# Kernel optimization log

Measured on AMD Instinct MI355X. Metric: run time of the kernel, lower is better.

The kernel has to match this reference:

```python
import jax, jax.numpy as jnp
import numpy as np


def setup_inputs() -> dict:
    key = jax.random.key(0)
    k1, k2 = jax.random.split(key)
    img_render_points = jax.random.normal(k1, (128, 128, 2), dtype=jnp.float32)
    ref_catheter_contour_point_cloud = jax.random.normal(k2, (16384, 2), dtype=jnp.float32)
    return {
        "img_render_points": img_render_points,
        "ref_catheter_contour_point_cloud": ref_catheter_contour_point_cloud,
    }


def reference(img_render_points, ref_catheter_contour_point_cloud):
    # Flatten to point cloud (N, 2)
    pc = img_render_points.reshape(-1, 2)
    ref = ref_catheter_contour_point_cloud  # (M, 2)
    # Pairwise Euclidean distances (N, M); torch.norm(..., dim=2) equivalent
    diff = pc[:, None, :] - ref[None, :, :]          # (N, M, 2)
    distances = jnp.sqrt(jnp.sum(diff * diff, axis=-1))  # (N, M)
    min_d1 = jnp.min(distances, axis=1)  # nearest ref point for each render point
    min_d2 = jnp.min(distances, axis=0)  # nearest render point for each ref point
    chamfer_loss = jnp.sum(min_d1) + jnp.sum(min_d2)
    return chamfer_loss
```

## Files before the change

### kernel.cpp

```cpp
#include <hip/hip_runtime.h>
#include <math.h>

#define NPTS 16384
#define G    64
#define NB   (G * G)
#define CAP  128
#define OCAP 2048
#define BV   5.0f
#define H    0.15625f
#define INVH (1.0f / H)
#define SLICE 1160


__global__ __launch_bounds__(256) void k_zero(unsigned int* __restrict__ cnt,
                                              float* __restrict__ out) {
    int i = blockIdx.x * 256 + threadIdx.x;
    if (i < 2 * NB + 2) cnt[i] = 0u;
    if (i == 0) out[0] = 0.0f;
}

__global__ __launch_bounds__(256) void k_scatter(
        const float2* __restrict__ pc, const float2* __restrict__ ref,
        unsigned int* __restrict__ cnt, unsigned int* __restrict__ ovf_cnt,
        float2* __restrict__ binned, float2* __restrict__ ovf) {
    int t  = blockIdx.x * 256 + threadIdx.x;
    int cl = t >> 14;
    int i  = t & (NPTS - 1);
    float2 p = (cl ? ref : pc)[i];
    int bx = (int)floorf((p.x + BV) * INVH); bx = min(max(bx, 0), G - 1);
    int by = (int)floorf((p.y + BV) * INVH); by = min(max(by, 0), G - 1);
    int b = cl * NB + by * G + bx;
    unsigned idx = atomicAdd(&cnt[b], 1u);
    if (idx < CAP) {
        binned[(size_t)b * CAP + idx] = p;
    } else {
        unsigned oi = atomicAdd(&ovf_cnt[cl], 1u);
        if (oi < OCAP) ovf[cl * OCAP + oi] = p;
    }
}

__global__ __launch_bounds__(256) void k_query(
        const float2* __restrict__ pc, const float2* __restrict__ ref,
        const unsigned int* __restrict__ cnt, const unsigned int* __restrict__ ovf_cnt,
        const float2* __restrict__ binned, const float2* __restrict__ ovf,
        float* __restrict__ out) {
    __shared__ float2 s_pts[4 * SLICE];
    __shared__ float  s_bsum[4];

    int d    = blockIdx.y;
    int td   = 1 - d;
    int wave = threadIdx.x >> 6;
    int lane = threadIdx.x & 63;
    int w    = blockIdx.x * 4 + wave;
    float2* my = s_pts + wave * SLICE;
    float sum = 0.0f;

    if (w < NB) {
        int c  = (w * 65) & (NB - 1);
        int cx = c & (G - 1), cy = c >> 6;
        int nq = (int)min(cnt[d * NB + c], (unsigned)CAP);
        if (nq > 0) {
            const unsigned int* tcnt = cnt + td * NB;
            const float2* tbin = binned + (size_t)td * NB * CAP;
            unsigned novf = min(ovf_cnt[td], (unsigned)OCAP);

            int nt = 0;
#pragma unroll
            for (int dy = -1; dy <= 1; ++dy) {
#pragma unroll
                for (int dx = -1; dx <= 1; ++dx) {
                    int x = cx + dx, y = cy + dy;
                    if ((unsigned)x < G && (unsigned)y < G) {
                        int t  = y * G + x;
                        int tn = (int)min(tcnt[t], (unsigned)CAP);
                        for (int i = lane; i < tn; i += 64)
                            my[nt + i] = tbin[(size_t)t * CAP + i];
                        nt += tn;
                    }
                }
            }
            int ntr = (nt + 3) & ~3;
            if (lane < ntr - nt) my[nt + lane] = make_float2(1e30f, 1e30f);

            for (int base = 0; base < nq; base += 64) {
                bool valid = (base + lane) < nq;
                float2 q = valid ? binned[((size_t)(d * NB + c)) * CAP + base + lane]
                                 : make_float2(0.0f, 0.0f);
                float best = valid ? INFINITY : 0.0f;

                for (unsigned j = 0; j < novf; ++j) {
                    float2 tp = ovf[td * OCAP + j];
                    float ddx = q.x - tp.x, ddy = q.y - tp.y;
                    best = fminf(best, fmaf(ddx, ddx, ddy * ddy));
                }

                const float4* p4 = (const float4*)my;
#pragma unroll 4
                for (int k = 0; k < ntr; k += 4) {
                    float4 ab = p4[k >> 1];
                    float4 cd = p4[(k >> 1) + 1];
                    float dx0 = q.x - ab.x, dy0 = q.y - ab.y;
                    float dx1 = q.x - ab.z, dy1 = q.y - ab.w;
                    float dx2 = q.x - cd.x, dy2 = q.y - cd.y;
                    float dx3 = q.x - cd.z, dy3 = q.y - cd.w;
                    float d0 = fmaf(dx0, dx0, dy0 * dy0);
                    float d1 = fmaf(dx1, dx1, dy1 * dy1);
                    float d2 = fmaf(dx2, dx2, dy2 * dy2);
                    float d3 = fmaf(dx3, dx3, dy3 * dy3);
                    best = fminf(best, fminf(fminf(d0, d1), fminf(d2, d3)));
                }

                for (int r = 2; r < G; ++r) {
                    float bnd = (float)(r - 1) * H;
                    if (__all(best <= bnd * bnd)) break;
                    int ncells = 8 * r;
                    for (int k0 = 0; k0 < ncells; k0 += 64) {
                        int k = k0 + lane;
                        int t = 0, tn = 0;
                        if (k < ncells) {
                            int side = (k >= 6 * r) ? 3 : (k >= 4 * r) ? 2 :
                                       (k >= 2 * r) ? 1 : 0;
                            int i = k - side * 2 * r;
                            int x, y;
                            if      (side == 0) { y = cy - r; x = cx - r + i; }
                            else if (side == 1) { x = cx + r; y = cy - r + i; }
                            else if (side == 2) { y = cy + r; x = cx + r - i; }
                            else                { x = cx - r; y = cy + r - i; }
                            if ((unsigned)x < G && (unsigned)y < G) {
                                t  = y * G + x;
                                tn = (int)min(tcnt[t], (unsigned)CAP);
                            }
                        }
                        unsigned long long mask = __ballot(tn > 0);
                        while (mask) {
                            int src = __builtin_ctzll(mask);
                            mask &= mask - 1;
                            int tt  = __shfl(t,  src, 64);
                            int ttn = __shfl(tn, src, 64);
                            const float2* tp = tbin + (size_t)tt * CAP;
                            for (int j = 0; j < ttn; ++j) {
                                float2 pt = tp[j];
                                float ddx = q.x - pt.x, ddy = q.y - pt.y;
                                best = fminf(best, fmaf(ddx, ddx, ddy * ddy));
                            }
                        }
                    }
                }
                if (valid) sum += sqrtf(best);
            }
        }
    } else if (w == NB) {
        unsigned n = min(ovf_cnt[d], (unsigned)OCAP);
        const float2* tgt = d ? pc : ref;
        for (unsigned i = lane; i < n; i += 64) {
            float2 q = ovf[d * OCAP + i];
            float best = INFINITY;
            for (int j = 0; j < NPTS; ++j) {
                float2 tp = tgt[j];
                float ddx = q.x - tp.x, ddy = q.y - tp.y;
                best = fminf(best, fmaf(ddx, ddx, ddy * ddy));
            }
            sum += sqrtf(best);
        }
    }

#pragma unroll
    for (int off = 32; off > 0; off >>= 1)
        sum += __shfl_down(sum, off, 64);
    if (lane == 0) s_bsum[wave] = sum;
    __syncthreads();
    if (threadIdx.x == 0) {
        float t = s_bsum[0] + s_bsum[1] + s_bsum[2] + s_bsum[3];
        if (t != 0.0f) atomicAdd(out, t);
    }
}

extern "C" void kernel_launch(void* const* d_in, const int* in_sizes, int n_in,
                              void* d_out, int out_size, void* d_ws, size_t ws_size,
                              hipStream_t stream) {
    const float2* pc  = (const float2*)d_in[0];
    const float2* ref = (const float2*)d_in[1];
    float* out = (float*)d_out;

    char* w = (char*)d_ws;
    unsigned int* cnt     = (unsigned int*)(w);
    unsigned int* ovf_cnt = (unsigned int*)(w + 32768);
    float2*       binned  = (float2*)(w + 65536);
    float2*       ovf     = (float2*)(w + 65536 +
                              (size_t)2 * NB * CAP * sizeof(float2));

    k_zero<<<(2 * NB + 2 + 255) / 256, 256, 0, stream>>>(cnt, out);
    k_scatter<<<(2 * NPTS) / 256, 256, 0, stream>>>(pc, ref, cnt, ovf_cnt, binned, ovf);
    k_query<<<dim3(1025, 2), 256, 0, stream>>>(pc, ref, cnt, ovf_cnt, binned, ovf, out);
}
```

Baseline: 102.6 us.

## Process two query points per lane and stage ring cells into LDS

Measured after the change: 88.86 us. 1.15x faster.

```diff
diff --git a/kernel.cpp b/kernel.cpp
--- a/kernel.cpp
+++ b/kernel.cpp
@@ -10,6 +10,7 @@
 #define H    0.15625f
 #define INVH (1.0f / H)
 #define SLICE 1160
+#define WCAP  1152
 
 
 __global__ __launch_bounds__(256) void k_zero(unsigned int* __restrict__ cnt,
@@ -64,90 +65,116 @@
             const float2* tbin = binned + (size_t)td * NB * CAP;
             unsigned novf = min(ovf_cnt[td], (unsigned)OCAP);
 
-            int nt = 0;
-#pragma unroll
-            for (int dy = -1; dy <= 1; ++dy) {
+            int tid9[9], tn9[9], nv = 0;
+#pragma unroll
+            for (int dy = -1; dy <= 1; ++dy)
 #pragma unroll
                 for (int dx = -1; dx <= 1; ++dx) {
                     int x = cx + dx, y = cy + dy;
                     if ((unsigned)x < G && (unsigned)y < G) {
-                        int t  = y * G + x;
-                        int tn = (int)min(tcnt[t], (unsigned)CAP);
-                        for (int i = lane; i < tn; i += 64)
-                            my[nt + i] = tbin[(size_t)t * CAP + i];
-                        nt += tn;
+                        tid9[nv] = y * G + x;
+                        tn9[nv]  = (int)min(tcnt[y * G + x], (unsigned)CAP);
+                        ++nv;
                     }
                 }
+            int nt = 0;
+            for (int v = 0; v < nv; ++v) {
+                int t = tid9[v], tn = tn9[v];
+                for (int i = lane; i < tn; i += 64)
+                    my[nt + i] = tbin[(size_t)t * CAP + i];
+                nt += tn;
             }
             int ntr = (nt + 3) & ~3;
             if (lane < ntr - nt) my[nt + lane] = make_float2(1e30f, 1e30f);
 
-            for (int base = 0; base < nq; base += 64) {
-                bool valid = (base + lane) < nq;
-                float2 q = valid ? binned[((size_t)(d * NB + c)) * CAP + base + lane]
-                                 : make_float2(0.0f, 0.0f);
-                float best = valid ? INFINITY : 0.0f;
-
-                for (unsigned j = 0; j < novf; ++j) {
-                    float2 tp = ovf[td * OCAP + j];
-                    float ddx = q.x - tp.x, ddy = q.y - tp.y;
-                    best = fminf(best, fmaf(ddx, ddx, ddy * ddy));
-                }
-
+            bool v0 = lane < nq, v1 = (64 + lane) < nq;
+            const float2* qbin = binned + (size_t)(d * NB + c) * CAP;
+            float2 q0 = qbin[lane];
+            float2 q1 = qbin[64 + lane];
+            float b0 = v0 ? INFINITY : 0.0f;
+            float b1 = v1 ? INFINITY : 0.0f;
+
+            for (unsigned j = 0; j < novf; ++j) {
+                float2 tp = ovf[td * OCAP + j];
+                float ax = q0.x - tp.x, ay = q0.y - tp.y;
+                float bx = q1.x - tp.x, by = q1.y - tp.y;
+                b0 = fminf(b0, fmaf(ax, ax, ay * ay));
+                b1 = fminf(b1, fmaf(bx, bx, by * by));
+            }
+
+            auto scan_lds = [&](int n4) {
                 const float4* p4 = (const float4*)my;
 #pragma unroll 4
-                for (int k = 0; k < ntr; k += 4) {
+                for (int k = 0; k < n4; k += 4) {
                     float4 ab = p4[k >> 1];
                     float4 cd = p4[(k >> 1) + 1];
-                    float dx0 = q.x - ab.x, dy0 = q.y - ab.y;
-                    float dx1 = q.x - ab.z, dy1 = q.y - ab.w;
-                    float dx2 = q.x - cd.x, dy2 = q.y - cd.y;
-                    float dx3 = q.x - cd.z, dy3 = q.y - cd.w;
-                    float d0 = fmaf(dx0, dx0, dy0 * dy0);
-                    float d1 = fmaf(dx1, dx1, dy1 * dy1);
-                    float d2 = fmaf(dx2, dx2, dy2 * dy2);
-                    float d3 = fmaf(dx3, dx3, dy3 * dy3);
-                    best = fminf(best, fminf(fminf(d0, d1), fminf(d2, d3)));
+                    float x0 = q0.x - ab.x, y0 = q0.y - ab.y;
+                    float x1 = q0.x - ab.z, y1 = q0.y - ab.w;
+                    float x2 = q0.x - cd.x, y2 = q0.y - cd.y;
+                    float x3 = q0.x - cd.z, y3 = q0.y - cd.w;
+                    float d0 = fmaf(x0, x0, y0 * y0);
+                    float d1 = fmaf(x1, x1, y1 * y1);
+                    float d2 = fmaf(x2, x2, y2 * y2);
+                    float d3 = fmaf(x3, x3, y3 * y3);
+                    b0 = fminf(b0, fminf(fminf(d0, d1), fminf(d2, d3)));
+                    float u0 = q1.x - ab.x, w0 = q1.y - ab.y;
+                    float u1 = q1.x - ab.z, w1 = q1.y - ab.w;
+                    float u2 = q1.x - cd.x, w2 = q1.y - cd.y;
+                    float u3 = q1.x - cd.z, w3 = q1.y - cd.w;
+                    float e0 = fmaf(u0, u0, w0 * w0);
+                    float e1 = fmaf(u1, u1, w1 * w1);
+                    float e2 = fmaf(u2, u2, w2 * w2);
+                    float e3 = fmaf(u3, u3, w3 * w3);
+                    b1 = fminf(b1, fminf(fminf(e0, e1), fminf(e2, e3)));
                 }
-
-                for (int r = 2; r < G; ++r) {
-                    float bnd = (float)(r - 1) * H;
-                    if (__all(best <= bnd * bnd)) break;
-                    int ncells = 8 * r;
-                    for (int k0 = 0; k0 < ncells; k0 += 64) {
-                        int k = k0 + lane;
-                        int t = 0, tn = 0;
-                        if (k < ncells) {
-                            int side = (k >= 6 * r) ? 3 : (k >= 4 * r) ? 2 :
-                                       (k >= 2 * r) ? 1 : 0;
-                            int i = k - side * 2 * r;
-                            int x, y;
-                            if      (side == 0) { y = cy - r; x = cx - r + i; }
-                            else if (side == 1) { x = cx + r; y = cy - r + i; }
-                            else if (side == 2) { y = cy + r; x = cx + r - i; }
-                            else                { x = cx - r; y = cy + r - i; }
-                            if ((unsigned)x < G && (unsigned)y < G) {
-                                t  = y * G + x;
-                                tn = (int)min(tcnt[t], (unsigned)CAP);
-                            }
+            };
+
+            scan_lds(ntr);
+
+            for (int r = 2; r < G; ++r) {
+                float bnd = (float)(r - 1) * H;
+                if (__all(fmaxf(b0, b1) <= bnd * bnd)) break;
+                int ncells = 8 * r;
+                for (int k0 = 0; k0 < ncells; k0 += 64) {
+                    int k = k0 + lane;
+                    int t = 0, tn = 0;
+                    if (k < ncells) {
+                        int side = (k >= 6 * r) ? 3 : (k >= 4 * r) ? 2 :
+                                   (k >= 2 * r) ? 1 : 0;
+                        int i = k - side * 2 * r;
+                        int x, y;
+                        if      (side == 0) { y = cy - r; x = cx - r + i; }
+                        else if (side == 1) { x = cx + r; y = cy - r + i; }
+                        else if (side == 2) { y = cy + r; x = cx + r - i; }
+                        else                { x = cx - r; y = cy + r - i; }
+                        if ((unsigned)x < G && (unsigned)y < G) {
+                            t  = y * G + x;
+                            tn = (int)min(tcnt[t], (unsigned)CAP);
                         }
-                        unsigned long long mask = __ballot(tn > 0);
-                        while (mask) {
-                            int src = __builtin_ctzll(mask);
-                            mask &= mask - 1;
-                            int tt  = __shfl(t,  src, 64);
-                            int ttn = __shfl(tn, src, 64);
-                            const float2* tp = tbin + (size_t)tt * CAP;
-                            for (int j = 0; j < ttn; ++j) {
-                                float2 pt = tp[j];
-                                float ddx = q.x - pt.x, ddy = q.y - pt.y;
-                                best = fminf(best, fmaf(ddx, ddx, ddy * ddy));
-                            }
+                    }
+                    int incl = tn;
+#pragma unroll
+                    for (int s = 1; s < 64; s <<= 1) {
+                        int o = __shfl_up(incl, s, 64);
+                        if (lane >= s) incl += o;
+                    }
+                    int off   = incl - tn;
+                    int total = __shfl(incl, 63, 64);
+                    for (int start = 0; start < total; start += WCAP) {
+                        int wend = min(total, start + WCAP);
+                        int wn   = wend - start;
+                        for (int j = 0; j < tn; ++j) {
+                            int g = off + j;
+                            if (g >= start && g < wend)
+                                my[g - start] = tbin[(size_t)t * CAP + j];
                         }
+                        int wnr = (wn + 3) & ~3;
+                        if (lane < wnr - wn) my[wn + lane] = make_float2(1e30f, 1e30f);
+                        scan_lds(wnr);
                     }
                 }
-                if (valid) sum += sqrtf(best);
-            }
+            }
+            sum = (v0 ? sqrtf(b0) : 0.0f) + (v1 ? sqrtf(b1) : 0.0f);
         }
     } else if (w == NB) {
         unsigned n = min(ovf_cnt[d], (unsigned)OCAP);
```
